# Optimization experiments

Measured on AMD Instinct MI355X. Metric: run time of the kernel, lower is better.

## Reference

```python
import jax, jax.numpy as jnp
import numpy as np

MOMENTUM = 0.01  # scalar momentum, init kwarg; trainable=False, initialization='unbiased', causal=True


def _ema_scan(x, m):
    """y[t] = (1-m)*y[t-1] + m*x[t], y[-1]=0, via log-depth associative scan over last axis."""
    a = jnp.full_like(x, 1.0 - m)
    b = m * x

    def combine(c1, c2):
        a1, b1 = c1
        a2, b2 = c2
        return a1 * a2, a2 * b1 + b2

    _, y = jax.lax.associative_scan(combine, (a, b), axis=-1)
    return y


def _bias_correction(num_samples, m, dtype):
    # correction[t] = 1 / (1 - (1-m)^(t+1)), t = 0..T-1
    power = jnp.arange(1, 1 + num_samples, dtype=dtype)
    return 1.0 / (1.0 - jnp.power(jnp.asarray(1.0 - m, dtype=dtype), power))


def setup_inputs() -> dict:
    key = jax.random.key(0)
    x = jax.random.normal(key, (32, 256, 8192), dtype=jnp.float32)
    return {"x": x}


def reference(x) -> jnp.ndarray:
    T = x.shape[-1]
    y = _ema_scan(x, MOMENTUM)
    corr = _bias_correction(T, MOMENTUM, x.dtype)  # [T], broadcasts over leading dims
    return y * corr
```

## Files before the change

kernel.cpp:

```cpp
#include <hip/hip_runtime.h>


namespace {

constexpr int T = 8192;
constexpr int BLOCK = 256;
constexpr int CHUNK = T / BLOCK;
constexpr int NWAVE = BLOCK / 64;
constexpr int V4 = T / 4;
constexpr int VPT = V4 / BLOCK;

__device__ __forceinline__ int sw4(int v) { return v ^ ((v >> 3) & 7); }

__global__ __launch_bounds__(BLOCK, 5) void ema_kernel(const float* __restrict__ x,
                                                       float* __restrict__ out) {
  __shared__ float4 sm4[V4];

  const int tid = threadIdx.x;
  const long long base = (long long)blockIdx.x * (long long)T;

  const float4* xv = reinterpret_cast<const float4*>(x + base);
#pragma unroll
  for (int k = 0; k < VPT; ++k) {
    const int slot = tid + BLOCK * k;
    const int g = sw4(slot);
    __builtin_amdgcn_global_load_lds(
        (const __attribute__((address_space(1))) void*)(xv + g),
        (__attribute__((address_space(3))) void*)(sm4 + slot), 16, 0, 0);
  }
  asm volatile("s_waitcnt vmcnt(0)" ::: "memory");
  __syncthreads();

  constexpr float A1 = 0.99f, M = 0.01f;
  constexpr float A2 = A1 * A1;
  constexpr float A4 = A2 * A2;
  constexpr float A8 = A4 * A4;
  constexpr float A16 = A8 * A8;
  constexpr float A32 = A16 * A16;
  constexpr float A64 = A32 * A32;
  constexpr float A128 = A64 * A64;
  constexpr float A256 = A128 * A128;
  constexpr float A512 = A256 * A256;
  constexpr float A1024 = A512 * A512;
  constexpr float A2048 = A1024 * A1024;

  const int vbase = tid * VPT;
  float acc[CHUNK];
  float run = 0.0f;
#pragma unroll
  for (int e4 = 0; e4 < VPT; ++e4) {
    const float4 v = sm4[sw4(vbase + e4)];
    run = fmaf(run, A1, M * v.x); acc[4 * e4 + 0] = run;
    run = fmaf(run, A1, M * v.y); acc[4 * e4 + 1] = run;
    run = fmaf(run, A1, M * v.z); acc[4 * e4 + 2] = run;
    run = fmaf(run, A1, M * v.w); acc[4 * e4 + 3] = run;
  }

  const int lane = tid & 63;
  const int w = tid >> 6;

  float S = run;
  {
    float t;
    t = __shfl_up(S, 1, 64);  if (lane >= 1)  S = fmaf(t, A32,   S);
    t = __shfl_up(S, 2, 64);  if (lane >= 2)  S = fmaf(t, A64,   S);
    t = __shfl_up(S, 4, 64);  if (lane >= 4)  S = fmaf(t, A128,  S);
    t = __shfl_up(S, 8, 64);  if (lane >= 8)  S = fmaf(t, A256,  S);
    t = __shfl_up(S, 16, 64); if (lane >= 16) S = fmaf(t, A512,  S);
    t = __shfl_up(S, 32, 64); if (lane >= 32) S = fmaf(t, A1024, S);
  }
  const float Sprev = __shfl_up(S, 1, 64);

  __syncthreads();
  float* smW = reinterpret_cast<float*>(sm4);
  if (lane == 63) smW[w] = S;
  __syncthreads();

  float Q = 0.0f;
#pragma unroll
  for (int v = 0; v < NWAVE - 1; ++v) {
    if (v < w) Q = fmaf(Q, A2048, smW[v]);
  }

  float Dlane = 1.0f;
  if (lane & 1)  Dlane *= A32;
  if (lane & 2)  Dlane *= A64;
  if (lane & 4)  Dlane *= A128;
  if (lane & 8)  Dlane *= A256;
  if (lane & 16) Dlane *= A512;
  if (lane & 32) Dlane *= A1024;

  const float carry = (lane ? Sprev : 0.0f) + Dlane * Q;

  float4* ov = reinterpret_cast<float4*>(out + base);
  float pw = 1.0f;

  if (w == 0) {
    float Pt = 1.0f;
    if (tid & 1)  Pt *= A32;
    if (tid & 2)  Pt *= A64;
    if (tid & 4)  Pt *= A128;
    if (tid & 8)  Pt *= A256;
    if (tid & 16) Pt *= A512;
    if (tid & 32) Pt *= A1024;
#pragma unroll
    for (int e4 = 0; e4 < VPT; ++e4) {
      float4 o;
      pw *= A1; Pt *= A1;
      o.x = fmaf(carry, pw, acc[4 * e4 + 0]) * __builtin_amdgcn_rcpf(1.0f - Pt);
      pw *= A1; Pt *= A1;
      o.y = fmaf(carry, pw, acc[4 * e4 + 1]) * __builtin_amdgcn_rcpf(1.0f - Pt);
      pw *= A1; Pt *= A1;
      o.z = fmaf(carry, pw, acc[4 * e4 + 2]) * __builtin_amdgcn_rcpf(1.0f - Pt);
      pw *= A1; Pt *= A1;
      o.w = fmaf(carry, pw, acc[4 * e4 + 3]) * __builtin_amdgcn_rcpf(1.0f - Pt);
      ov[vbase + e4] = o;
    }
  } else {
#pragma unroll
    for (int e4 = 0; e4 < VPT; ++e4) {
      float4 o;
      pw *= A1; o.x = fmaf(carry, pw, acc[4 * e4 + 0]);
      pw *= A1; o.y = fmaf(carry, pw, acc[4 * e4 + 1]);
      pw *= A1; o.z = fmaf(carry, pw, acc[4 * e4 + 2]);
      pw *= A1; o.w = fmaf(carry, pw, acc[4 * e4 + 3]);
      ov[vbase + e4] = o;
    }
  }
}

}

extern "C" void kernel_launch(void* const* d_in, const int* in_sizes, int n_in,
                              void* d_out, int out_size, void* d_ws, size_t ws_size,
                              hipStream_t stream) {
  const float* x = (const float*)d_in[0];
  float* out = (float*)d_out;
  const int rows = in_sizes[0] / T;
  ema_kernel<<<dim3(rows), dim3(BLOCK), 0, stream>>>(x, out);
}
```

Before: 441.6 us.

## Process one row per wave with double-buffered segment DMA and carried scan

Each wavefront now owns a whole row and walks it in 1024-element segments. It double-buffers global-to-LDS DMA loads so the next segment's fetch overlaps the current segment's scan. The prefix carry moves between segments through a cross-lane shuffle, which removes the block-wide barriers and shared-memory wave-carry exchange. Outputs are staged back through LDS so the global stores stay coalesced. In exchange, each wave has less memory in flight at once, and the code relies on implicit waits for the asynchronous LDS loads, which could race.

```diff
diff --git a/kernel.cpp b/kernel.cpp
--- a/kernel.cpp
+++ b/kernel.cpp
@@ -5,31 +5,28 @@
 
 constexpr int T = 8192;
 constexpr int BLOCK = 256;
-constexpr int CHUNK = T / BLOCK;
-constexpr int NWAVE = BLOCK / 64;
-constexpr int V4 = T / 4;
-constexpr int VPT = V4 / BLOCK;
+constexpr int WPB = BLOCK / 64;
+constexpr int SEGV = 256;
+constexpr int NSEG = T / (4 * SEGV);
 
-__device__ __forceinline__ int sw4(int v) { return v ^ ((v >> 3) & 7); }
+__device__ __forceinline__ int sw4(int s) { return s ^ ((s >> 3) & 7); }
+
+__device__ __forceinline__ void dma16(const float4* g, float4* l) {
+  __builtin_amdgcn_global_load_lds(
+      (const __attribute__((address_space(1))) void*)g,
+      (__attribute__((address_space(3))) void*)l, 16, 0, 0);
+}
 
 __global__ __launch_bounds__(BLOCK, 5) void ema_kernel(const float* __restrict__ x,
                                                        float* __restrict__ out) {
-  __shared__ float4 sm4[V4];
+  __shared__ float4 sm4[WPB][2][SEGV];
 
   const int tid = threadIdx.x;
-  const long long base = (long long)blockIdx.x * (long long)T;
-
-  const float4* xv = reinterpret_cast<const float4*>(x + base);
-#pragma unroll
-  for (int k = 0; k < VPT; ++k) {
-    const int slot = tid + BLOCK * k;
-    const int g = sw4(slot);
-    __builtin_amdgcn_global_load_lds(
-        (const __attribute__((address_space(1))) void*)(xv + g),
-        (__attribute__((address_space(3))) void*)(sm4 + slot), 16, 0, 0);
-  }
-  asm volatile("s_waitcnt vmcnt(0)" ::: "memory");
-  __syncthreads();
+  const int lane = tid & 63;
+  const int w = tid >> 6;
+  const long long row = (long long)blockIdx.x * WPB + w;
+  const float4* xv = reinterpret_cast<const float4*>(x) + row * (T / 4);
+  float4* ov = reinterpret_cast<float4*>(out) + row * (T / 4);
 
   constexpr float A1 = 0.99f, M = 0.01f;
   constexpr float A2 = A1 * A1;
@@ -42,89 +39,122 @@
   constexpr float A256 = A128 * A128;
   constexpr float A512 = A256 * A256;
   constexpr float A1024 = A512 * A512;
-  constexpr float A2048 = A1024 * A1024;
 
-  const int vbase = tid * VPT;
-  float acc[CHUNK];
-  float run = 0.0f;
+  float Dlane = 1.0f;
+  if (lane & 1)  Dlane *= A16;
+  if (lane & 2)  Dlane *= A32;
+  if (lane & 4)  Dlane *= A64;
+  if (lane & 8)  Dlane *= A128;
+  if (lane & 16) Dlane *= A256;
+  if (lane & 32) Dlane *= A512;
+
 #pragma unroll
-  for (int e4 = 0; e4 < VPT; ++e4) {
-    const float4 v = sm4[sw4(vbase + e4)];
-    run = fmaf(run, A1, M * v.x); acc[4 * e4 + 0] = run;
-    run = fmaf(run, A1, M * v.y); acc[4 * e4 + 1] = run;
-    run = fmaf(run, A1, M * v.z); acc[4 * e4 + 2] = run;
-    run = fmaf(run, A1, M * v.w); acc[4 * e4 + 3] = run;
+  for (int k = 0; k < 4; ++k) {
+    const int slot = lane + 64 * k;
+    dma16(xv + sw4(slot), &sm4[w][0][slot]);
   }
 
-  const int lane = tid & 63;
-  const int w = tid >> 6;
+  float c_in = 0.0f;
 
-  float S = run;
-  {
-    float t;
-    t = __shfl_up(S, 1, 64);  if (lane >= 1)  S = fmaf(t, A32,   S);
-    t = __shfl_up(S, 2, 64);  if (lane >= 2)  S = fmaf(t, A64,   S);
-    t = __shfl_up(S, 4, 64);  if (lane >= 4)  S = fmaf(t, A128,  S);
-    t = __shfl_up(S, 8, 64);  if (lane >= 8)  S = fmaf(t, A256,  S);
-    t = __shfl_up(S, 16, 64); if (lane >= 16) S = fmaf(t, A512,  S);
-    t = __shfl_up(S, 32, 64); if (lane >= 32) S = fmaf(t, A1024, S);
-  }
-  const float Sprev = __shfl_up(S, 1, 64);
+#pragma unroll
+  for (int s = 0; s < NSEG; ++s) {
+    const int b = s & 1;
 
-  __syncthreads();
-  float* smW = reinterpret_cast<float*>(sm4);
-  if (lane == 63) smW[w] = S;
-  __syncthreads();
+    const float4 f0 = sm4[w][b][sw4(4 * lane + 0)];
+    const float4 f1 = sm4[w][b][sw4(4 * lane + 1)];
+    const float4 f2 = sm4[w][b][sw4(4 * lane + 2)];
+    const float4 f3 = sm4[w][b][sw4(4 * lane + 3)];
 
-  float Q = 0.0f;
+    if (s + 1 < NSEG) {
 #pragma unroll
-  for (int v = 0; v < NWAVE - 1; ++v) {
-    if (v < w) Q = fmaf(Q, A2048, smW[v]);
-  }
+      for (int k = 0; k < 4; ++k) {
+        const int slot = lane + 64 * k;
+        dma16(xv + (s + 1) * SEGV + sw4(slot), &sm4[w][b ^ 1][slot]);
+      }
+    }
 
-  float Dlane = 1.0f;
-  if (lane & 1)  Dlane *= A32;
-  if (lane & 2)  Dlane *= A64;
-  if (lane & 4)  Dlane *= A128;
-  if (lane & 8)  Dlane *= A256;
-  if (lane & 16) Dlane *= A512;
-  if (lane & 32) Dlane *= A1024;
+    float acc[16];
+    float run = 0.0f;
+    run = fmaf(run, A1, M * f0.x); acc[0]  = run;
+    run = fmaf(run, A1, M * f0.y); acc[1]  = run;
+    run = fmaf(run, A1, M * f0.z); acc[2]  = run;
+    run = fmaf(run, A1, M * f0.w); acc[3]  = run;
+    run = fmaf(run, A1, M * f1.x); acc[4]  = run;
+    run = fmaf(run, A1, M * f1.y); acc[5]  = run;
+    run = fmaf(run, A1, M * f1.z); acc[6]  = run;
+    run = fmaf(run, A1, M * f1.w); acc[7]  = run;
+    run = fmaf(run, A1, M * f2.x); acc[8]  = run;
+    run = fmaf(run, A1, M * f2.y); acc[9]  = run;
+    run = fmaf(run, A1, M * f2.z); acc[10] = run;
+    run = fmaf(run, A1, M * f2.w); acc[11] = run;
+    run = fmaf(run, A1, M * f3.x); acc[12] = run;
+    run = fmaf(run, A1, M * f3.y); acc[13] = run;
+    run = fmaf(run, A1, M * f3.z); acc[14] = run;
+    run = fmaf(run, A1, M * f3.w); acc[15] = run;
 
-  const float carry = (lane ? Sprev : 0.0f) + Dlane * Q;
+    float S = run;
+    {
+      float t;
+      t = __shfl_up(S, 1, 64);  if (lane >= 1)  S = fmaf(t, A16,  S);
+      t = __shfl_up(S, 2, 64);  if (lane >= 2)  S = fmaf(t, A32,  S);
+      t = __shfl_up(S, 4, 64);  if (lane >= 4)  S = fmaf(t, A64,  S);
+      t = __shfl_up(S, 8, 64);  if (lane >= 8)  S = fmaf(t, A128, S);
+      t = __shfl_up(S, 16, 64); if (lane >= 16) S = fmaf(t, A256, S);
+      t = __shfl_up(S, 32, 64); if (lane >= 32) S = fmaf(t, A512, S);
+    }
+    const float Sprev = __shfl_up(S, 1, 64);
 
-  float4* ov = reinterpret_cast<float4*>(out + base);
-  float pw = 1.0f;
+    const float carry = (lane ? Sprev : 0.0f) + Dlane * c_in;
+    c_in = __shfl(S, 63, 64) + A1024 * c_in;
 
-  if (w == 0) {
-    float Pt = 1.0f;
-    if (tid & 1)  Pt *= A32;
-    if (tid & 2)  Pt *= A64;
-    if (tid & 4)  Pt *= A128;
-    if (tid & 8)  Pt *= A256;
-    if (tid & 16) Pt *= A512;
-    if (tid & 32) Pt *= A1024;
+    float4 y0, y1, y2, y3;
+    float pw = 1.0f;
+    if (s < 2) {
+      float Pt = (s == 1) ? Dlane * A1024 : Dlane;
+      pw *= A1; Pt *= A1; y0.x = fmaf(carry, pw, acc[0])  * __builtin_amdgcn_rcpf(1.0f - Pt);
+      pw *= A1; Pt *= A1; y0.y = fmaf(carry, pw, acc[1])  * __builtin_amdgcn_rcpf(1.0f - Pt);
+      pw *= A1; Pt *= A1; y0.z = fmaf(carry, pw, acc[2])  * __builtin_amdgcn_rcpf(1.0f - Pt);
+      pw *= A1; Pt *= A1; y0.w = fmaf(carry, pw, acc[3])  * __builtin_amdgcn_rcpf(1.0f - Pt);
+      pw *= A1; Pt *= A1; y1.x = fmaf(carry, pw, acc[4])  * __builtin_amdgcn_rcpf(1.0f - Pt);
+      pw *= A1; Pt *= A1; y1.y = fmaf(carry, pw, acc[5])  * __builtin_amdgcn_rcpf(1.0f - Pt);
+      pw *= A1; Pt *= A1; y1.z = fmaf(carry, pw, acc[6])  * __builtin_amdgcn_rcpf(1.0f - Pt);
+      pw *= A1; Pt *= A1; y1.w = fmaf(carry, pw, acc[7])  * __builtin_amdgcn_rcpf(1.0f - Pt);
+      pw *= A1; Pt *= A1; y2.x = fmaf(carry, pw, acc[8])  * __builtin_amdgcn_rcpf(1.0f - Pt);
+      pw *= A1; Pt *= A1; y2.y = fmaf(carry, pw, acc[9])  * __builtin_amdgcn_rcpf(1.0f - Pt);
+      pw *= A1; Pt *= A1; y2.z = fmaf(carry, pw, acc[10]) * __builtin_amdgcn_rcpf(1.0f - Pt);
+      pw *= A1; Pt *= A1; y2.w = fmaf(carry, pw, acc[11]) * __builtin_amdgcn_rcpf(1.0f - Pt);
+      pw *= A1; Pt *= A1; y3.x = fmaf(carry, pw, acc[12]) * __builtin_amdgcn_rcpf(1.0f - Pt);
+      pw *= A1; Pt *= A1; y3.y = fmaf(carry, pw, acc[13]) * __builtin_amdgcn_rcpf(1.0f - Pt);
+      pw *= A1; Pt *= A1; y3.z = fmaf(carry, pw, acc[14]) * __builtin_amdgcn_rcpf(1.0f - Pt);
+      pw *= A1; Pt *= A1; y3.w = fmaf(carry, pw, acc[15]) * __builtin_amdgcn_rcpf(1.0f - Pt);
+    } else {
+      pw *= A1; y0.x = fmaf(carry, pw, acc[0]);
+      pw *= A1; y0.y = fmaf(carry, pw, acc[1]);
+      pw *= A1; y0.z = fmaf(carry, pw, acc[2]);
+      pw *= A1; y0.w = fmaf(carry, pw, acc[3]);
+      pw *= A1; y1.x = fmaf(carry, pw, acc[4]);
+      pw *= A1; y1.y = fmaf(carry, pw, acc[5]);
+      pw *= A1; y1.z = fmaf(carry, pw, acc[6]);
+      pw *= A1; y1.w = fmaf(carry, pw, acc[7]);
+      pw *= A1; y2.x = fmaf(carry, pw, acc[8]);
+      pw *= A1; y2.y = fmaf(carry, pw, acc[9]);
+      pw *= A1; y2.z = fmaf(carry, pw, acc[10]);
+      pw *= A1; y2.w = fmaf(carry, pw, acc[11]);
+      pw *= A1; y3.x = fmaf(carry, pw, acc[12]);
+      pw *= A1; y3.y = fmaf(carry, pw, acc[13]);
+      pw *= A1; y3.z = fmaf(carry, pw, acc[14]);
+      pw *= A1; y3.w = fmaf(carry, pw, acc[15]);
+    }
+
+    sm4[w][b][sw4(4 * lane + 0)] = y0;
+    sm4[w][b][sw4(4 * lane + 1)] = y1;
+    sm4[w][b][sw4(4 * lane + 2)] = y2;
+    sm4[w][b][sw4(4 * lane + 3)] = y3;
+
 #pragma unroll
-    for (int e4 = 0; e4 < VPT; ++e4) {
-      float4 o;
-      pw *= A1; Pt *= A1;
-      o.x = fmaf(carry, pw, acc[4 * e4 + 0]) * __builtin_amdgcn_rcpf(1.0f - Pt);
-      pw *= A1; Pt *= A1;
-      o.y = fmaf(carry, pw, acc[4 * e4 + 1]) * __builtin_amdgcn_rcpf(1.0f - Pt);
-      pw *= A1; Pt *= A1;
-      o.z = fmaf(carry, pw, acc[4 * e4 + 2]) * __builtin_amdgcn_rcpf(1.0f - Pt);
-      pw *= A1; Pt *= A1;
-      o.w = fmaf(carry, pw, acc[4 * e4 + 3]) * __builtin_amdgcn_rcpf(1.0f - Pt);
-      ov[vbase + e4] = o;
-    }
-  } else {
-#pragma unroll
-    for (int e4 = 0; e4 < VPT; ++e4) {
-      float4 o;
-      pw *= A1; o.x = fmaf(carry, pw, acc[4 * e4 + 0]);
-      pw *= A1; o.y = fmaf(carry, pw, acc[4 * e4 + 1]);
-      pw *= A1; o.z = fmaf(carry, pw, acc[4 * e4 + 2]);
-      pw *= A1; o.w = fmaf(carry, pw, acc[4 * e4 + 3]);
-      ov[vbase + e4] = o;
+    for (int k = 0; k < 4; ++k) {
+      const int u = lane + 64 * k;
+      ov[s * SEGV + u] = sm4[w][b][sw4(u)];
     }
   }
 }
@@ -137,5 +167,5 @@
   const float* x = (const float*)d_in[0];
   float* out = (float*)d_out;
   const int rows = in_sizes[0] / T;
-  ema_kernel<<<dim3(rows), dim3(BLOCK), 0, stream>>>(x, out);
+  ema_kernel<<<dim3(rows / WPB), dim3(BLOCK), 0, stream>>>(x, out);
 }
```

Result: faster. 429.5 us (-2.7%).
